# Optimization experiments

Measured on AMD Instinct MI355X. Metric: run time of the kernel, lower is better.

## Reference

```python
import jax, jax.numpy as jnp
import numpy as np

N, E, B = 100000, 400000, 1024
NF, EF, H, C, D = 32, 16, 256, 256, 6
LN_EPS = 1e-5


def setup_inputs() -> dict:
    key = jax.random.key(0)
    ks = jax.random.split(key, 32)
    def nrm(k, shape, s=0.05):
        return jax.random.normal(k, shape, jnp.float32) * s
    inp = {}
    inp['node_x'] = jax.random.normal(ks[0], (N, NF), jnp.float32)
    inp['edge_e'] = jax.random.normal(ks[1], (E, EF), jnp.float32)
    inp['t'] = jax.random.uniform(ks[2], (B,), jnp.float32)
    inp['n_index'] = jnp.sort(jax.random.randint(ks[3], (N,), 0, B))
    inp['src'] = jax.random.randint(ks[4], (E,), 0, N)
    inp['dst'] = jax.random.randint(ks[5], (E,), 0, N)
    inp['in_conv_w'] = nrm(ks[6], (NF, H), 0.1)
    inp['in_conv_b'] = jnp.zeros((H,), jnp.float32)
    inp['edge_w'] = nrm(ks[7], (EF, H), 0.1)
    inp['edge_b'] = jnp.zeros((H,), jnp.float32)
    inp['t_w1'] = nrm(ks[8], (128, C))
    inp['t_b1'] = jnp.zeros((C,), jnp.float32)
    inp['t_w2'] = nrm(ks[9], (C, C))
    inp['t_b2'] = jnp.zeros((C,), jnp.float32)
    inp['conv1_w'] = nrm(ks[10], (D, H, H))
    inp['conv1_b'] = jnp.zeros((D, H), jnp.float32)
    inp['conv2_w'] = nrm(ks[11], (D, H, H))
    inp['conv2_b'] = jnp.zeros((D, H), jnp.float32)
    inp['ln1_g'] = jnp.ones((D, H), jnp.float32)
    inp['ln1_b'] = jnp.zeros((D, H), jnp.float32)
    inp['ln2_g'] = jnp.ones((D, H), jnp.float32)
    inp['ln2_b'] = jnp.zeros((D, H), jnp.float32)
    inp['film1_w'] = nrm(ks[12], (D, C, 2 * H))
    inp['film1_b'] = nrm(ks[13], (D, 2 * H), 0.01)
    inp['film2_w'] = nrm(ks[14], (D, C, 2 * H))
    inp['film2_b'] = nrm(ks[15], (D, 2 * H), 0.01)
    # NOTE: source zero-inits the head; we use small random weights so the
    # baseline output is non-degenerate (init detail, not forward math).
    inp['head_w'] = nrm(ks[16], (H, 1))
    inp['head_b'] = jnp.zeros((1,), jnp.float32)
    return inp


def reference(node_x, edge_e, t, n_index, src, dst,
              in_conv_w, in_conv_b, edge_w, edge_b,
              t_w1, t_b1, t_w2, t_b2,
              conv1_w, conv1_b, conv2_w, conv2_b,
              ln1_g, ln1_b, ln2_g, ln2_b,
              film1_w, film1_b, film2_w, film2_b,
              head_w, head_b):
    n = node_x.shape[0]
    b = t.shape[0]
    ones_e = jnp.ones(src.shape[0], node_x.dtype)
    # DGL GraphConv norm='both': D_dst^{-1/2} A (D_src^{-1/2} X) W + b, degrees clamped to >=1
    deg_out = jnp.clip(jax.ops.segment_sum(ones_e, src, num_segments=n), 1.0)
    deg_in = jnp.clip(jax.ops.segment_sum(ones_e, dst, num_segments=n), 1.0)
    no = deg_out ** -0.5
    ni = deg_in ** -0.5

    def gconv(x, W, bia):
        agg = jax.ops.segment_sum((x * no[:, None])[src], dst, num_segments=n)
        return (agg * ni[:, None]) @ W + bia

    def lnorm(x, g, bia):
        mu = jnp.mean(x, -1, keepdims=True)
        v = jnp.mean(jnp.square(x - mu), -1, keepdims=True)
        return (x - mu) * jax.lax.rsqrt(v + LN_EPS) * g + bia

    def film(x, cond, fw, fb):
        gb = cond @ fw + fb           # (B, 2H)
        gam, bet = jnp.split(gb, 2, axis=-1)
        return x * (1.0 + gam[n_index]) + bet[n_index]

    # sinusoidal time embedding + MLP
    half = t_w1.shape[0] // 2
    freqs = jnp.exp(-jnp.log(1000.0) * jnp.arange(half, dtype=jnp.float32) / half)
    a = (t * 1000.0)[:, None] * freqs[None, :]
    emb = jnp.concatenate([jnp.sin(a), jnp.cos(a)], axis=-1)   # (B, 128)
    cond = jax.nn.silu(emb @ t_w1 + t_b1) @ t_w2 + t_b2        # (B, C)

    h = gconv(node_x, in_conv_w, in_conv_b)                    # (N, H)
    e_h = edge_e @ edge_w + edge_b                             # (E, H)
    e_mean = jax.ops.segment_sum(e_h, dst, num_segments=n) / deg_in[:, None]
    h = h + e_mean

    for i in range(conv1_w.shape[0]):
        # NOTE: source module has a bug: conv2 consumes the block INPUT (not the
        # conv1 branch), so the conv1/norm1/film1/silu result is dead. Replicated
        # faithfully; jit DCEs the dead branch.
        _dead = jax.nn.silu(film(lnorm(gconv(h, conv1_w[i], conv1_b[i]), ln1_g[i], ln1_b[i]), cond, film1_w[i], film1_b[i]))
        h2 = jax.nn.silu(film(lnorm(gconv(h, conv2_w[i], conv2_b[i]), ln2_g[i], ln2_b[i]), cond, film2_w[i], film2_b[i]))
        h = h2 + h  # skip = Identity since in_dim == out_dim

    ones_n = jnp.ones(n, h.dtype)
    cnt = jnp.clip(jax.ops.segment_sum(ones_n, n_index, num_segments=b), 1.0)
    g_mean = jax.ops.segment_sum(h, n_index, num_segments=b) / cnt[:, None]
    return g_mean @ head_w + head_b  # scale = 1.0
```

## Files before the change

### kernel.cpp

```cpp
#include <hip/hip_runtime.h>
#include <math.h>

#define HDIM 256
#define NLAYERS 6

typedef __attribute__((ext_vector_type(8))) short short8v;
typedef __attribute__((ext_vector_type(16))) float f32x16;

__device__ __forceinline__ float silu_(float x){ return x * (1.f/(1.f+__expf(-x))); }

__device__ __forceinline__ unsigned short f2bf(float f){
  unsigned u = __float_as_uint(f);
  u += 0x7FFF + ((u>>16)&1);
  return (unsigned short)(u>>16);
}
__device__ __forceinline__ float bf2f(unsigned short b){ return __uint_as_float(((unsigned)b)<<16); }

__device__ __forceinline__ void gload_lds16(const void* g, void* l){
  __builtin_amdgcn_global_load_lds((const __attribute__((address_space(1))) void*)g,
                                   (__attribute__((address_space(3))) void*)l, 16, 0, 0);
}

__global__ void k_count(const int* __restrict__ src, const int* __restrict__ dst, int E,
                        int* __restrict__ cnt_out, int* __restrict__ cnt_in){
  int e = blockIdx.x*256 + threadIdx.x;
  if(e < E){
    atomicAdd(&cnt_out[src[e]], 1);
    atomicAdd(&cnt_in[dst[e]], 1);
  }
}

__global__ __launch_bounds__(256) void k_scan1(const int* __restrict__ cnt_in,
                                               int* __restrict__ partial, int N){
  __shared__ int s[256];
  int b = blockIdx.x, tid = threadIdx.x;
  int i0 = b*1024 + tid*4;
  int sum = 0;
  #pragma unroll
  for(int j=0;j<4;j++){ int i=i0+j; if(i<N) sum += cnt_in[i]; }
  s[tid] = sum; __syncthreads();
  for(int off=128; off; off>>=1){ if(tid<off) s[tid]+=s[tid+off]; __syncthreads(); }
  if(tid==0) partial[b] = s[0];
}
__global__ __launch_bounds__(256) void k_scan2(int* __restrict__ partial,
                                               int* __restrict__ csr_off, int nb, int N){
  __shared__ int s[256];
  int tid = threadIdx.x;
  int v = (tid<nb) ? partial[tid] : 0;
  s[tid] = v; __syncthreads();
  for(int off=1; off<256; off<<=1){
    int t = (tid>=off) ? s[tid-off] : 0;
    __syncthreads(); s[tid] += t; __syncthreads();
  }
  if(tid<nb) partial[tid] = s[tid] - v;
  if(tid==255) csr_off[N] = s[255];
}
__global__ __launch_bounds__(256) void k_scan3(const int* __restrict__ cnt_in,
                                               const int* __restrict__ partial,
                                               int* __restrict__ csr_off, int N){
  __shared__ int s[256];
  int b = blockIdx.x, tid = threadIdx.x;
  int i0 = b*1024 + tid*4;
  int c[4];
  #pragma unroll
  for(int j=0;j<4;j++){ int i=i0+j; c[j] = (i<N) ? cnt_in[i] : 0; }
  int tot = c[0]+c[1]+c[2]+c[3];
  s[tid] = tot; __syncthreads();
  for(int off=1; off<256; off<<=1){
    int t = (tid>=off) ? s[tid-off] : 0;
    __syncthreads(); s[tid] += t; __syncthreads();
  }
  int run = s[tid] - tot + partial[b];
  #pragma unroll
  for(int j=0;j<4;j++){
    int i = i0+j;
    if(i<N) csr_off[i] = run;
    run += c[j];
  }
}

__global__ void k_prep(const int* __restrict__ cnt_out, const int* __restrict__ cnt_in,
                       const int* __restrict__ csr_off, const int* __restrict__ n_index,
                       float* __restrict__ no, float* __restrict__ ni,
                       int* __restrict__ csr_pos, int* __restrict__ gcnt, int N){
  int v = blockIdx.x*256 + threadIdx.x;
  if(v < N){
    no[v] = rsqrtf((float)max(cnt_out[v],1));
    ni[v] = rsqrtf((float)max(cnt_in[v],1));
    csr_pos[v] = csr_off[v];
    atomicAdd(&gcnt[n_index[v]], 1);
  }
}

__global__ void k_fill(const int* __restrict__ src, const int* __restrict__ dst, int E,
                       int* __restrict__ csr_pos, int* __restrict__ csr_src,
                       int* __restrict__ csr_eid){
  int e = blockIdx.x*256 + threadIdx.x;
  if(e < E){
    int p = atomicAdd(&csr_pos[dst[e]], 1);
    csr_src[p] = src[e];
    csr_eid[p] = e;
  }
}

__global__ __launch_bounds__(256) void k_cond(const float* __restrict__ t,
        const float* __restrict__ w1, const float* __restrict__ b1,
        const float* __restrict__ w2, const float* __restrict__ b2,
        float* __restrict__ cond){
  __shared__ float emb[128];
  __shared__ float hid[256];
  int b = blockIdx.x, tid = threadIdx.x;
  float tv = t[b] * 1000.f;
  if(tid < 128){
    int k = tid & 63;
    float fr = expf(-logf(1000.f) * (float)k * (1.f/64.f));
    float a = tv * fr;
    emb[tid] = (tid < 64) ? sinf(a) : cosf(a);
  }
  __syncthreads();
  {
    float s = b1[tid];
    for(int k=0;k<128;k++) s += emb[k] * w1[k*HDIM + tid];
    hid[tid] = silu_(s);
  }
  __syncthreads();
  {
    float s = b2[tid];
    for(int k=0;k<256;k++) s += hid[k] * w2[k*HDIM + tid];
    cond[(size_t)b*HDIM + tid] = s;
  }
}

template<int K>
__global__ __launch_bounds__(256) void k_gemm_f32(
    const float* __restrict__ A, int lda,
    const float* __restrict__ W, int ldw,
    const float* __restrict__ bias,
    float* __restrict__ out, int ldo, int M, int mode){
  if(mode == 1){
    int c = blockIdx.y;
    W    += (size_t)(c>>1)*131072 + (size_t)(c&1)*256;
    bias += (size_t)(c>>1)*512 + (size_t)(c&1)*256;
    out  += (size_t)c*1024*256;
  }
  __shared__ float As[64][36];
  __shared__ float Ws[32][256];
  const int tid = threadIdx.x;
  const int rg = tid >> 4;
  const int cg = tid & 15;
  const int row0 = blockIdx.x * 64;

  float4 acc[4][4];
  #pragma unroll
  for(int i=0;i<4;i++)
    #pragma unroll
    for(int m=0;m<4;m++) acc[i][m] = make_float4(0.f,0.f,0.f,0.f);

  const int ar = tid >> 2;
  const int ac = (tid & 3) * 8;
  const int wr = tid >> 3;
  const int wc = (tid & 7) * 32;

  for(int kk=0; kk<K; kk+=32){
    {
      int gr = row0 + ar;
      float4 v0 = make_float4(0.f,0.f,0.f,0.f), v1 = v0;
      if(gr < M){
        v0 = *(const float4*)&A[(size_t)gr*lda + kk + ac];
        v1 = *(const float4*)&A[(size_t)gr*lda + kk + ac + 4];
      }
      *(float4*)&As[ar][ac]   = v0;
      *(float4*)&As[ar][ac+4] = v1;
    }
    #pragma unroll
    for(int u=0;u<8;u++)
      *(float4*)&Ws[wr][wc + u*4] = *(const float4*)&W[(size_t)(kk+wr)*ldw + wc + u*4];
    __syncthreads();
    #pragma unroll 8
    for(int k=0;k<32;k++){
      float a0 = As[rg*4+0][k];
      float a1 = As[rg*4+1][k];
      float a2 = As[rg*4+2][k];
      float a3 = As[rg*4+3][k];
      #pragma unroll
      for(int m=0;m<4;m++){
        float4 w = *(const float4*)&Ws[k][cg*4 + m*64];
        acc[0][m].x += a0*w.x; acc[0][m].y += a0*w.y; acc[0][m].z += a0*w.z; acc[0][m].w += a0*w.w;
        acc[1][m].x += a1*w.x; acc[1][m].y += a1*w.y; acc[1][m].z += a1*w.z; acc[1][m].w += a1*w.w;
        acc[2][m].x += a2*w.x; acc[2][m].y += a2*w.y; acc[2][m].z += a2*w.z; acc[2][m].w += a2*w.w;
        acc[3][m].x += a3*w.x; acc[3][m].y += a3*w.y; acc[3][m].z += a3*w.z; acc[3][m].w += a3*w.w;
      }
    }
    __syncthreads();
  }

  const int c0 = cg * 4;
  #pragma unroll
  for(int i=0;i<4;i++){
    const int gr = row0 + rg*4 + i;
    if(gr >= M) continue;
    #pragma unroll
    for(int m=0;m<4;m++){
      const int c = c0 + m*64;
      float4 b4 = *(const float4*)&bias[c];
      float4 o = make_float4(acc[i][m].x+b4.x, acc[i][m].y+b4.y,
                             acc[i][m].z+b4.z, acc[i][m].w+b4.w);
      *(float4*)&out[(size_t)gr*ldo + c] = o;
    }
  }
}

__global__ void k_wcat(const float* __restrict__ in_w, const float* __restrict__ ew,
                       const float* __restrict__ eb, float* __restrict__ wcat){
  int idx = blockIdx.x*256 + threadIdx.x;
  int r = idx>>8, c = idx&255;
  float v = 0.f;
  if(r < 32) v = in_w[r*HDIM + c];
  else if(r < 48) v = ew[(r-32)*HDIM + c];
  else if(r == 48) v = eb[c];
  wcat[idx] = v;
}

__global__ void k_w2b(const float* __restrict__ W, unsigned short* __restrict__ hi_,
                      unsigned short* __restrict__ lo_){
  int idx = blockIdx.x*256 + threadIdx.x;
  int i = idx >> 16, r = idx & 65535;
  int n = r >> 8, k = r & 255;
  float v = W[((size_t)i*256 + k)*256 + n];
  unsigned short h = f2bf(v);
  float lo = v - bf2f(h);
  hi_[((size_t)i*256 + n)*256 + k] = h;
  lo_[((size_t)i*256 + n)*256 + k] = f2bf(lo);
}

__global__ __launch_bounds__(256) void k_init_agg(const float* __restrict__ node_x,
    const float* __restrict__ edge_e,
    const int* __restrict__ csr_off, const int* __restrict__ csr_src, const int* __restrict__ csr_eid,
    const float* __restrict__ no, const float* __restrict__ ni, const int* __restrict__ cnt_in,
    float* __restrict__ A48, int N){
  int v = blockIdx.x*4 + (threadIdx.x>>6);
  if(v >= N) return;
  int lane = threadIdx.x & 63;
  int beg = csr_off[v], end = csr_off[v+1];
  float acc = 0.f;
  for(int p=beg; p<end; p++){
    int s = csr_src[p]; int e = csr_eid[p];
    if(lane < 32)      acc += node_x[(size_t)s*32 + lane] * no[s];
    else if(lane < 48) acc += edge_e[(size_t)e*16 + (lane-32)];
  }
  int ci = cnt_in[v];
  float out;
  if(lane < 32)      out = acc * ni[v];
  else if(lane < 48) out = acc * (1.f/(float)max(ci,1));
  else if(lane == 48) out = (ci>0) ? 1.f : 0.f;
  else out = 0.f;
  A48[(size_t)v*64 + lane] = out;
}

__global__ __launch_bounds__(256) void k_gather_bf(const float* __restrict__ h,
   const int* __restrict__ csr_off, const int* __restrict__ csr_src,
   const float* __restrict__ no, const float* __restrict__ ni,
   unsigned short* __restrict__ ahi, int N, int Npad){
  int v = blockIdx.x*4 + (threadIdx.x>>6);
  if(v >= Npad) return;
  int lane = threadIdx.x & 63;
  float4 acc = make_float4(0.f,0.f,0.f,0.f);
  if(v < N){
    int beg = csr_off[v], end = csr_off[v+1];
    for(int p=beg; p<end; p++){
      int s = csr_src[p];
      float w = no[s];
      float4 x = *(const float4*)&h[(size_t)s*HDIM + lane*4];
      acc.x += x.x*w; acc.y += x.y*w; acc.z += x.z*w; acc.w += x.w*w;
    }
    float sc = ni[v];
    acc.x*=sc; acc.y*=sc; acc.z*=sc; acc.w*=sc;
  }
  ushort4 hv = make_ushort4(f2bf(acc.x), f2bf(acc.y), f2bf(acc.z), f2bf(acc.w));
  *(ushort4*)&ahi[(size_t)v*HDIM + lane*4] = hv;
}

template<bool LAST>
__global__ __launch_bounds__(256, 2) void k_layer_mfma(
    const unsigned short* __restrict__ Ahi,
    const unsigned short* __restrict__ Bhi, const unsigned short* __restrict__ Blo,
    const float* __restrict__ bias, const float* __restrict__ lng, const float* __restrict__ lnb,
    const float* __restrict__ gamL, const float* __restrict__ betL,
    const int* __restrict__ n_index, float* __restrict__ h,
    const float* __restrict__ hw, float* __restrict__ gsum, int N){
  __shared__ __align__(16) char smem[65536];
  unsigned short* AsH = (unsigned short*)smem;
  float* zbuf = (float*)smem;
  const int tid = threadIdx.x;
  const int w = tid >> 6, l = tid & 63;
  const int half = l >> 5, lcol = l & 31;
  const int row0 = blockIdx.x * 64;
  const int colb = w * 64;

  const size_t bb = (size_t)(colb + lcol)*HDIM + half*8;

  short8v Bh0[4], Bh1[4], Bl0[4], Bl1[4];
  #define LOADB(t, s) { \
    Bh0[s] = *(const short8v*)&Bhi[bb + (t)*16]; \
    Bh1[s] = *(const short8v*)&Bhi[bb + 32*HDIM + (t)*16]; \
    Bl0[s] = *(const short8v*)&Blo[bb + (t)*16]; \
    Bl1[s] = *(const short8v*)&Blo[bb + 32*HDIM + (t)*16]; }
  LOADB(0,0) LOADB(1,1) LOADB(2,2)

  {
    const int m = tid & 31;
    const int rofs = tid >> 5;
    #pragma unroll
    for(int chunk=0; chunk<8; chunk++){
      const int row = chunk*8 + rofs;
      const int msw = (m & 24) | ((m ^ row) & 7);
      const size_t src = (size_t)(row0 + row)*HDIM + msw*8;
      gload_lds16(&Ahi[src], (char*)smem + chunk*4096 + tid*16);
    }
  }
  __syncthreads();

  f32x16 acc[2][2] = {};
  const char* baseH = (const char*)smem;

  #pragma unroll
  for(int t=0; t<16; t++){
    if(t < 13) LOADB(t+3, (t+3)&3)
    const int s = t & 3;
    const int g = t*2 + half;
    const int slot = (g & 24) | ((g ^ lcol) & 7);
    short8v ah0 = *(const short8v*)(baseH + lcol*512 + slot*16);
    short8v ah1 = *(const short8v*)(baseH + (32+lcol)*512 + slot*16);

    acc[0][0] = __builtin_amdgcn_mfma_f32_32x32x16_bf16(ah0, Bh0[s], acc[0][0], 0,0,0);
    acc[0][1] = __builtin_amdgcn_mfma_f32_32x32x16_bf16(ah0, Bh1[s], acc[0][1], 0,0,0);
    acc[1][0] = __builtin_amdgcn_mfma_f32_32x32x16_bf16(ah1, Bh0[s], acc[1][0], 0,0,0);
    acc[1][1] = __builtin_amdgcn_mfma_f32_32x32x16_bf16(ah1, Bh1[s], acc[1][1], 0,0,0);
    acc[0][0] = __builtin_amdgcn_mfma_f32_32x32x16_bf16(ah0, Bl0[s], acc[0][0], 0,0,0);
    acc[0][1] = __builtin_amdgcn_mfma_f32_32x32x16_bf16(ah0, Bl1[s], acc[0][1], 0,0,0);
    acc[1][0] = __builtin_amdgcn_mfma_f32_32x32x16_bf16(ah1, Bl0[s], acc[1][0], 0,0,0);
    acc[1][1] = __builtin_amdgcn_mfma_f32_32x32x16_bf16(ah1, Bl1[s], acc[1][1], 0,0,0);
  }
  #undef LOADB

  float bias_c[2];
  bias_c[0] = bias[colb + lcol];
  bias_c[1] = bias[colb + 32 + lcol];
  __syncthreads();
  #pragma unroll
  for(int mt=0; mt<2; mt++){
    #pragma unroll
    for(int r=0; r<16; r++){
      const int rl = (r&3) + 8*(r>>2) + 4*half;
      const int row = mt*32 + rl;
      zbuf[row*HDIM + colb      + lcol] = acc[mt][0][r] + bias_c[0];
      zbuf[row*HDIM + colb + 32 + lcol] = acc[mt][1][r] + bias_c[1];
    }
  }
  __syncthreads();

  const float4 lng4 = *(const float4*)&lng[l*4];
  const float4 lnb4 = *(const float4*)&lnb[l*4];
  float4 hw4;
  if(LAST) hw4 = *(const float4*)&hw[l*4];
  #pragma unroll
  for(int rr=0; rr<16; rr++){
    const int row = w*16 + rr;
    const int grow = row0 + row;
    const bool ok = grow < N;
    float4 z4 = *(const float4*)&zbuf[row*HDIM + l*4];
    float s = z4.x + z4.y + z4.z + z4.w;
    float q = z4.x*z4.x + z4.y*z4.y + z4.z*z4.z + z4.w*z4.w;
    #pragma unroll
    for(int off=1; off<64; off<<=1){ s += __shfl_xor(s, off, 64); q += __shfl_xor(q, off, 64); }
    const float mu = s * (1.f/256.f);
    const float rs = rsqrtf(fmaxf(q*(1.f/256.f) - mu*mu, 0.f) + 1e-5f);
    const int bidx = ok ? n_index[grow] : 0;
    const float4 gam4 = *(const float4*)&gamL[(size_t)bidx*HDIM + l*4];
    const float4 bet4 = *(const float4*)&betL[(size_t)bidx*HDIM + l*4];
    float4 o;
    { float zn=(z4.x-mu)*rs*lng4.x+lnb4.x; o.x=silu_(zn*(1.f+gam4.x)+bet4.x); }
    { float zn=(z4.y-mu)*rs*lng4.y+lnb4.y; o.y=silu_(zn*(1.f+gam4.y)+bet4.y); }
    { float zn=(z4.z-mu)*rs*lng4.z+lnb4.z; o.z=silu_(zn*(1.f+gam4.z)+bet4.z); }
    { float zn=(z4.w-mu)*rs*lng4.w+lnb4.w; o.w=silu_(zn*(1.f+gam4.w)+bet4.w); }
    if(LAST){
      float4 hv = ok ? *(const float4*)&h[(size_t)grow*HDIM + l*4]
                     : make_float4(0.f,0.f,0.f,0.f);
      float rd = (o.x+hv.x)*hw4.x + (o.y+hv.y)*hw4.y + (o.z+hv.z)*hw4.z + (o.w+hv.w)*hw4.w;
      #pragma unroll
      for(int off=1; off<64; off<<=1) rd += __shfl_xor(rd, off, 64);
      if(l == 0 && ok) atomicAdd(&gsum[bidx], rd);
    } else {
      if(ok){
        float4 hv = *(const float4*)&h[(size_t)grow*HDIM + l*4];
        o.x += hv.x; o.y += hv.y; o.z += hv.z; o.w += hv.w;
        *(float4*)&h[(size_t)grow*HDIM + l*4] = o;
      }
    }
  }
}

__global__ void k_final(const float* __restrict__ gsum, const int* __restrict__ gcnt,
                        const float* __restrict__ hb, float* __restrict__ out, int B){
  int b = blockIdx.x*256 + threadIdx.x;
  if(b < B) out[b] = gsum[b] / (float)max(gcnt[b],1) + hb[0];
}

extern "C" void kernel_launch(void* const* d_in, const int* in_sizes, int n_in,
                              void* d_out, int out_size, void* d_ws, size_t ws_size,
                              hipStream_t stream){
  const float* node_x   = (const float*)d_in[0];
  const float* edge_e   = (const float*)d_in[1];
  const float* t        = (const float*)d_in[2];
  const int*   n_index  = (const int*)d_in[3];
  const int*   src      = (const int*)d_in[4];
  const int*   dst      = (const int*)d_in[5];
  const float* in_conv_w= (const float*)d_in[6];
  const float* in_conv_b= (const float*)d_in[7];
  const float* edge_w   = (const float*)d_in[8];
  const float* edge_b   = (const float*)d_in[9];
  const float* t_w1     = (const float*)d_in[10];
  const float* t_b1     = (const float*)d_in[11];
  const float* t_w2     = (const float*)d_in[12];
  const float* t_b2     = (const float*)d_in[13];
  const float* conv2_w  = (const float*)d_in[16];
  const float* conv2_b  = (const float*)d_in[17];
  const float* ln2_g    = (const float*)d_in[20];
  const float* ln2_b    = (const float*)d_in[21];
  const float* film2_w  = (const float*)d_in[24];
  const float* film2_b  = (const float*)d_in[25];
  const float* head_w   = (const float*)d_in[26];
  const float* head_b   = (const float*)d_in[27];

  const int N = in_sizes[3];
  const int E = in_sizes[4];
  const int B = in_sizes[2];
  const int Npad = (N + 63) & ~63;

  char* w = (char*)d_ws;
  auto alloc = [&](size_t bytes)->char*{
    char* p = w; w += (bytes + 255) & ~(size_t)255; return p;
  };
  int*   cnt_out = (int*)  alloc((size_t)N*4);
  int*   cnt_in  = (int*)  alloc((size_t)N*4);
  float* no      = (float*)alloc((size_t)N*4);
  float* ni      = (float*)alloc((size_t)N*4);
  int*   csr_off = (int*)  alloc((size_t)(N+1)*4);
  int*   csr_pos = (int*)  alloc((size_t)N*4);
  int*   csr_src = (int*)  alloc((size_t)E*4);
  int*   csr_eid = (int*)  alloc((size_t)E*4);
  int*   partial = (int*)  alloc((size_t)256*4);
  float* cond    = (float*)alloc((size_t)B*HDIM*4);
  float* gbX     = (float*)alloc((size_t)12*B*HDIM*4);
  float* gsum    = (float*)alloc((size_t)B*4);
  int*   gcnt    = (int*)  alloc((size_t)B*4);
  float* h       = (float*)alloc((size_t)N*HDIM*4);
  unsigned short* agg_hi = (unsigned short*)alloc((size_t)Npad*HDIM*2);
  unsigned short* Wthi   = (unsigned short*)alloc((size_t)NLAYERS*HDIM*HDIM*2);
  unsigned short* Wtlo   = (unsigned short*)alloc((size_t)NLAYERS*HDIM*HDIM*2);
  float* wcat    = (float*)alloc((size_t)64*HDIM*4);
  float* A48     = (float*)alloc((size_t)Npad*64*4);

  hipMemsetAsync(cnt_out, 0, (size_t)N*4, stream);
  hipMemsetAsync(cnt_in,  0, (size_t)N*4, stream);
  hipMemsetAsync(gsum,    0, (size_t)B*4, stream);
  hipMemsetAsync(gcnt,    0, (size_t)B*4, stream);

  int gE = (E+255)/256, gN = (N+255)/256;
  int nb1 = (N+1023)/1024;
  k_count<<<gE,256,0,stream>>>(src, dst, E, cnt_out, cnt_in);
  k_scan1<<<nb1,256,0,stream>>>(cnt_in, partial, N);
  k_scan2<<<1,256,0,stream>>>(partial, csr_off, nb1, N);
  k_scan3<<<nb1,256,0,stream>>>(cnt_in, partial, csr_off, N);
  k_prep<<<gN,256,0,stream>>>(cnt_out, cnt_in, csr_off, n_index, no, ni, csr_pos, gcnt, N);
  k_fill<<<gE,256,0,stream>>>(src, dst, E, csr_pos, csr_src, csr_eid);

  k_cond<<<B,256,0,stream>>>(t, t_w1, t_b1, t_w2, t_b2, cond);
  k_gemm_f32<256><<<dim3(B/64,12),256,0,stream>>>(cond, HDIM, film2_w, 512, film2_b,
                                                  gbX, HDIM, B, 1);

  k_w2b<<<NLAYERS*HDIM*HDIM/256,256,0,stream>>>(conv2_w, Wthi, Wtlo);
  k_wcat<<<64,256,0,stream>>>(in_conv_w, edge_w, edge_b, wcat);
  k_init_agg<<<(N+3)/4,256,0,stream>>>(node_x, edge_e, csr_off, csr_src, csr_eid,
                                       no, ni, cnt_in, A48, N);
  k_gemm_f32<64><<<Npad/64,256,0,stream>>>(A48, 64, wcat, HDIM, in_conv_b, h, HDIM, N, 0);

  for(int i=0;i<NLAYERS;i++){
    k_gather_bf<<<Npad/4,256,0,stream>>>(h, csr_off, csr_src, no, ni, agg_hi, N, Npad);
    if(i < NLAYERS-1)
      k_layer_mfma<false><<<Npad/64,256,0,stream>>>(agg_hi,
          Wthi + (size_t)i*HDIM*HDIM, Wtlo + (size_t)i*HDIM*HDIM,
          conv2_b + (size_t)i*HDIM,
          ln2_g + (size_t)i*HDIM, ln2_b + (size_t)i*HDIM,
          gbX + (size_t)(2*i)*B*HDIM, gbX + (size_t)(2*i+1)*B*HDIM,
          n_index, h, head_w, gsum, N);
    else
      k_layer_mfma<true><<<Npad/64,256,0,stream>>>(agg_hi,
          Wthi + (size_t)i*HDIM*HDIM, Wtlo + (size_t)i*HDIM*HDIM,
          conv2_b + (size_t)i*HDIM,
          ln2_g + (size_t)i*HDIM, ln2_b + (size_t)i*HDIM,
          gbX + (size_t)(2*i)*B*HDIM, gbX + (size_t)(2*i+1)*B*HDIM,
          n_index, h, head_w, gsum, N);
  }

  k_final<<<(B+255)/256,256,0,stream>>>(gsum, gcnt, head_b, (float*)d_out, B);
}
```

Before: 1.505 ms.

## Keep a bf16 shadow of node features for gather and halve layer LDS

The layer and input GEMM kernels now also write a bf16 copy of the hidden state, and the neighbour gather reads that copy instead of fp32 rows. This halves the bytes fetched per edge in the gather-bound aggregation. The layer kernel's epilogue is split into two 32-row passes so LDS drops from 64KB to 32KB, and the occupancy hint is raised from 2 to 5 blocks. Aggregation inputs lose precision before the bf16 conversion they already went through, and the layer kernel writes an extra bf16 array.

Result: slower. 2.281 ms (+51.6%).

```diff
diff --git a/kernel.cpp b/kernel.cpp
--- a/kernel.cpp
+++ b/kernel.cpp
@@ -136,7 +136,8 @@
     const float* __restrict__ A, int lda,
     const float* __restrict__ W, int ldw,
     const float* __restrict__ bias,
-    float* __restrict__ out, int ldo, int M, int mode){
+    float* __restrict__ out, int ldo, int M, int mode,
+    unsigned short* __restrict__ out_bf){
   if(mode == 1){
     int c = blockIdx.y;
     W    += (size_t)(c>>1)*131072 + (size_t)(c&1)*256;
@@ -206,6 +207,9 @@
       float4 o = make_float4(acc[i][m].x+b4.x, acc[i][m].y+b4.y,
                              acc[i][m].z+b4.z, acc[i][m].w+b4.w);
       *(float4*)&out[(size_t)gr*ldo + c] = o;
+      if(out_bf)
+        *(ushort4*)&out_bf[(size_t)gr*ldo + c] =
+            make_ushort4(f2bf(o.x), f2bf(o.y), f2bf(o.z), f2bf(o.w));
     }
   }
 }
@@ -257,7 +261,7 @@
   A48[(size_t)v*64 + lane] = out;
 }
 
-__global__ __launch_bounds__(256) void k_gather_bf(const float* __restrict__ h,
+__global__ __launch_bounds__(256) void k_gather_bf(const unsigned short* __restrict__ hbf,
    const int* __restrict__ csr_off, const int* __restrict__ csr_src,
    const float* __restrict__ no, const float* __restrict__ ni,
    unsigned short* __restrict__ ahi, int N, int Npad){
@@ -270,8 +274,9 @@
     for(int p=beg; p<end; p++){
       int s = csr_src[p];
       float w = no[s];
-      float4 x = *(const float4*)&h[(size_t)s*HDIM + lane*4];
-      acc.x += x.x*w; acc.y += x.y*w; acc.z += x.z*w; acc.w += x.w*w;
+      ushort4 x = *(const ushort4*)&hbf[(size_t)s*HDIM + lane*4];
+      acc.x += bf2f(x.x)*w; acc.y += bf2f(x.y)*w;
+      acc.z += bf2f(x.z)*w; acc.w += bf2f(x.w)*w;
     }
     float sc = ni[v];
     acc.x*=sc; acc.y*=sc; acc.z*=sc; acc.w*=sc;
@@ -281,15 +286,15 @@
 }
 
 template<bool LAST>
-__global__ __launch_bounds__(256, 2) void k_layer_mfma(
+__global__ __launch_bounds__(256, 5) void k_layer_mfma(
     const unsigned short* __restrict__ Ahi,
     const unsigned short* __restrict__ Bhi, const unsigned short* __restrict__ Blo,
     const float* __restrict__ bias, const float* __restrict__ lng, const float* __restrict__ lnb,
     const float* __restrict__ gamL, const float* __restrict__ betL,
     const int* __restrict__ n_index, float* __restrict__ h,
+    unsigned short* __restrict__ hbf,
     const float* __restrict__ hw, float* __restrict__ gsum, int N){
-  __shared__ __align__(16) char smem[65536];
-  unsigned short* AsH = (unsigned short*)smem;
+  __shared__ __align__(16) char smem[32768];
   float* zbuf = (float*)smem;
   const int tid = threadIdx.x;
   const int w = tid >> 6, l = tid & 63;
@@ -346,55 +351,56 @@
   float bias_c[2];
   bias_c[0] = bias[colb + lcol];
   bias_c[1] = bias[colb + 32 + lcol];
-  __syncthreads();
-  #pragma unroll
-  for(int mt=0; mt<2; mt++){
-    #pragma unroll
-    for(int r=0; r<16; r++){
-      const int rl = (r&3) + 8*(r>>2) + 4*half;
-      const int row = mt*32 + rl;
-      zbuf[row*HDIM + colb      + lcol] = acc[mt][0][r] + bias_c[0];
-      zbuf[row*HDIM + colb + 32 + lcol] = acc[mt][1][r] + bias_c[1];
-    }
-  }
-  __syncthreads();
-
   const float4 lng4 = *(const float4*)&lng[l*4];
   const float4 lnb4 = *(const float4*)&lnb[l*4];
   float4 hw4;
   if(LAST) hw4 = *(const float4*)&hw[l*4];
-  #pragma unroll
-  for(int rr=0; rr<16; rr++){
-    const int row = w*16 + rr;
-    const int grow = row0 + row;
-    const bool ok = grow < N;
-    float4 z4 = *(const float4*)&zbuf[row*HDIM + l*4];
-    float s = z4.x + z4.y + z4.z + z4.w;
-    float q = z4.x*z4.x + z4.y*z4.y + z4.z*z4.z + z4.w*z4.w;
+
+  #pragma unroll
+  for(int pass=0; pass<2; pass++){
+    __syncthreads();
     #pragma unroll
-    for(int off=1; off<64; off<<=1){ s += __shfl_xor(s, off, 64); q += __shfl_xor(q, off, 64); }
-    const float mu = s * (1.f/256.f);
-    const float rs = rsqrtf(fmaxf(q*(1.f/256.f) - mu*mu, 0.f) + 1e-5f);
-    const int bidx = ok ? n_index[grow] : 0;
-    const float4 gam4 = *(const float4*)&gamL[(size_t)bidx*HDIM + l*4];
-    const float4 bet4 = *(const float4*)&betL[(size_t)bidx*HDIM + l*4];
-    float4 o;
-    { float zn=(z4.x-mu)*rs*lng4.x+lnb4.x; o.x=silu_(zn*(1.f+gam4.x)+bet4.x); }
-    { float zn=(z4.y-mu)*rs*lng4.y+lnb4.y; o.y=silu_(zn*(1.f+gam4.y)+bet4.y); }
-    { float zn=(z4.z-mu)*rs*lng4.z+lnb4.z; o.z=silu_(zn*(1.f+gam4.z)+bet4.z); }
-    { float zn=(z4.w-mu)*rs*lng4.w+lnb4.w; o.w=silu_(zn*(1.f+gam4.w)+bet4.w); }
-    if(LAST){
-      float4 hv = ok ? *(const float4*)&h[(size_t)grow*HDIM + l*4]
-                     : make_float4(0.f,0.f,0.f,0.f);
-      float rd = (o.x+hv.x)*hw4.x + (o.y+hv.y)*hw4.y + (o.z+hv.z)*hw4.z + (o.w+hv.w)*hw4.w;
+    for(int r=0; r<16; r++){
+      const int rl = (r&3) + 8*(r>>2) + 4*half;
+      zbuf[rl*HDIM + colb      + lcol] = acc[pass][0][r] + bias_c[0];
+      zbuf[rl*HDIM + colb + 32 + lcol] = acc[pass][1][r] + bias_c[1];
+    }
+    __syncthreads();
+    #pragma unroll
+    for(int rr=0; rr<8; rr++){
+      const int row = w*8 + rr;
+      const int grow = row0 + pass*32 + row;
+      const bool ok = grow < N;
+      float4 z4 = *(const float4*)&zbuf[row*HDIM + l*4];
+      float s = z4.x + z4.y + z4.z + z4.w;
+      float q = z4.x*z4.x + z4.y*z4.y + z4.z*z4.z + z4.w*z4.w;
       #pragma unroll
-      for(int off=1; off<64; off<<=1) rd += __shfl_xor(rd, off, 64);
-      if(l == 0 && ok) atomicAdd(&gsum[bidx], rd);
-    } else {
-      if(ok){
-        float4 hv = *(const float4*)&h[(size_t)grow*HDIM + l*4];
-        o.x += hv.x; o.y += hv.y; o.z += hv.z; o.w += hv.w;
-        *(float4*)&h[(size_t)grow*HDIM + l*4] = o;
+      for(int off=1; off<64; off<<=1){ s += __shfl_xor(s, off, 64); q += __shfl_xor(q, off, 64); }
+      const float mu = s * (1.f/256.f);
+      const float rs = rsqrtf(fmaxf(q*(1.f/256.f) - mu*mu, 0.f) + 1e-5f);
+      const int bidx = ok ? n_index[grow] : 0;
+      const float4 gam4 = *(const float4*)&gamL[(size_t)bidx*HDIM + l*4];
+      const float4 bet4 = *(const float4*)&betL[(size_t)bidx*HDIM + l*4];
+      float4 o;
+      { float zn=(z4.x-mu)*rs*lng4.x+lnb4.x; o.x=silu_(zn*(1.f+gam4.x)+bet4.x); }
+      { float zn=(z4.y-mu)*rs*lng4.y+lnb4.y; o.y=silu_(zn*(1.f+gam4.y)+bet4.y); }
+      { float zn=(z4.z-mu)*rs*lng4.z+lnb4.z; o.z=silu_(zn*(1.f+gam4.z)+bet4.z); }
+      { float zn=(z4.w-mu)*rs*lng4.w+lnb4.w; o.w=silu_(zn*(1.f+gam4.w)+bet4.w); }
+      if(LAST){
+        float4 hv = ok ? *(const float4*)&h[(size_t)grow*HDIM + l*4]
+                       : make_float4(0.f,0.f,0.f,0.f);
+        float rd = (o.x+hv.x)*hw4.x + (o.y+hv.y)*hw4.y + (o.z+hv.z)*hw4.z + (o.w+hv.w)*hw4.w;
+        #pragma unroll
+        for(int off=1; off<64; off<<=1) rd += __shfl_xor(rd, off, 64);
+        if(l == 0 && ok) atomicAdd(&gsum[bidx], rd);
+      } else {
+        if(ok){
+          float4 hv = *(const float4*)&h[(size_t)grow*HDIM + l*4];
+          o.x += hv.x; o.y += hv.y; o.z += hv.z; o.w += hv.w;
+          *(float4*)&h[(size_t)grow*HDIM + l*4] = o;
+          *(ushort4*)&hbf[(size_t)grow*HDIM + l*4] =
+              make_ushort4(f2bf(o.x), f2bf(o.y), f2bf(o.z), f2bf(o.w));
+        }
       }
     }
   }
@@ -455,6 +461,7 @@
   float* gsum    = (float*)alloc((size_t)B*4);
   int*   gcnt    = (int*)  alloc((size_t)B*4);
   float* h       = (float*)alloc((size_t)N*HDIM*4);
+  unsigned short* hbf    = (unsigned short*)alloc((size_t)Npad*HDIM*2);
   unsigned short* agg_hi = (unsigned short*)alloc((size_t)Npad*HDIM*2);
   unsigned short* Wthi   = (unsigned short*)alloc((size_t)NLAYERS*HDIM*HDIM*2);
   unsigned short* Wtlo   = (unsigned short*)alloc((size_t)NLAYERS*HDIM*HDIM*2);
@@ -477,30 +484,30 @@
 
   k_cond<<<B,256,0,stream>>>(t, t_w1, t_b1, t_w2, t_b2, cond);
   k_gemm_f32<256><<<dim3(B/64,12),256,0,stream>>>(cond, HDIM, film2_w, 512, film2_b,
-                                                  gbX, HDIM, B, 1);
+                                                  gbX, HDIM, B, 1, nullptr);
 
   k_w2b<<<NLAYERS*HDIM*HDIM/256,256,0,stream>>>(conv2_w, Wthi, Wtlo);
   k_wcat<<<64,256,0,stream>>>(in_conv_w, edge_w, edge_b, wcat);
   k_init_agg<<<(N+3)/4,256,0,stream>>>(node_x, edge_e, csr_off, csr_src, csr_eid,
                                        no, ni, cnt_in, A48, N);
-  k_gemm_f32<64><<<Npad/64,256,0,stream>>>(A48, 64, wcat, HDIM, in_conv_b, h, HDIM, N, 0);
+  k_gemm_f32<64><<<Npad/64,256,0,stream>>>(A48, 64, wcat, HDIM, in_conv_b, h, HDIM, N, 0, hbf);
 
   for(int i=0;i<NLAYERS;i++){
-    k_gather_bf<<<Npad/4,256,0,stream>>>(h, csr_off, csr_src, no, ni, agg_hi, N, Npad);
+    k_gather_bf<<<Npad/4,256,0,stream>>>(hbf, csr_off, csr_src, no, ni, agg_hi, N, Npad);
     if(i < NLAYERS-1)
       k_layer_mfma<false><<<Npad/64,256,0,stream>>>(agg_hi,
           Wthi + (size_t)i*HDIM*HDIM, Wtlo + (size_t)i*HDIM*HDIM,
           conv2_b + (size_t)i*HDIM,
           ln2_g + (size_t)i*HDIM, ln2_b + (size_t)i*HDIM,
           gbX + (size_t)(2*i)*B*HDIM, gbX + (size_t)(2*i+1)*B*HDIM,
-          n_index, h, head_w, gsum, N);
+          n_index, h, hbf, head_w, gsum, N);
     else
       k_layer_mfma<true><<<Npad/64,256,0,stream>>>(agg_hi,
           Wthi + (size_t)i*HDIM*HDIM, Wtlo + (size_t)i*HDIM*HDIM,
           conv2_b + (size_t)i*HDIM,
           ln2_g + (size_t)i*HDIM, ln2_b + (size_t)i*HDIM,
           gbX + (size_t)(2*i)*B*HDIM, gbX + (size_t)(2*i+1)*B*HDIM,
-          n_index, h, head_w, gsum, N);
+          n_index, h, hbf, head_w, gsum, N);
   }
 
   k_final<<<(B+255)/256,256,0,stream>>>(gsum, gcnt, head_b, (float*)d_out, B);
```
